# Kernel optimization log

Hardware: AMD Instinct MI355X
Metric: run time of the kernel (lower is better)

Reference implementation:

```python
import jax, jax.numpy as jnp
import numpy as np

V, D, B, S, T, MAXLEN = 32000, 256, 4, 512, 256, 512


def _gru(x, Wih, Whh, bih, bhh):
    """torch-style GRU over x:[B,L,Din] -> [B,L,D]. Weight rows ordered [r,z,n]."""
    Dh = Whh.shape[1]
    xW = x @ Wih.T + bih  # [B,L,3D] precompute input projections

    def step(h, xw):
        hW = h @ Whh.T + bhh
        xr, xz, xn = jnp.split(xw, 3, axis=-1)
        hr, hz, hn = jnp.split(hW, 3, axis=-1)
        r = jax.nn.sigmoid(xr + hr)
        z = jax.nn.sigmoid(xz + hz)
        n = jnp.tanh(xn + r * hn)
        h = (1.0 - z) * n + z * h
        return h, h

    h0 = jnp.zeros((x.shape[0], Dh), x.dtype)
    _, ys = jax.lax.scan(step, h0, jnp.swapaxes(xW, 0, 1))
    return jnp.swapaxes(ys, 0, 1)


def setup_inputs() -> dict:
    key = jax.random.key(0)
    ks = jax.random.split(key, 24)

    def n(k, shape, scale=0.02):
        return (jax.random.normal(k, shape, jnp.float32) * scale).astype(jnp.float32)

    inp = {
        "src": jax.random.randint(ks[0], (B, S), 0, V),
        "tgt": jax.random.randint(ks[1], (B, T), 0, V),
        "emb": n(ks[2], (V, D)),
        "pos": n(ks[3], (MAXLEN, D)),
        # encoder forward direction
        "ef_wih": n(ks[4], (3 * D, D)), "ef_whh": n(ks[5], (3 * D, D)),
        "ef_bih": n(ks[6], (3 * D,)), "ef_bhh": n(ks[7], (3 * D,)),
        # encoder backward direction
        "eb_wih": n(ks[8], (3 * D, D)), "eb_whh": n(ks[9], (3 * D, D)),
        "eb_bih": n(ks[10], (3 * D,)), "eb_bhh": n(ks[11], (3 * D,)),
        # decoder
        "d_wih": n(ks[12], (3 * D, D)), "d_whh": n(ks[13], (3 * D, D)),
        "d_bih": n(ks[14], (3 * D,)), "d_bhh": n(ks[15], (3 * D,)),
        "Wq": n(ks[16], (D, D)),
        "Wk": n(ks[17], (D, 2 * D)),
        "Wgen": n(ks[18], (V, 3 * D)), "bgen": n(ks[19], (V,)),
        "Wgate": n(ks[20], (1, 3 * D)), "bgate": n(ks[21], (1,)),
    }
    return inp


def reference(src, tgt, emb, pos,
              ef_wih, ef_whh, ef_bih, ef_bhh,
              eb_wih, eb_whh, eb_bih, eb_bhh,
              d_wih, d_whh, d_bih, d_bhh,
              Wq, Wk, Wgen, bgen, Wgate, bgate):
    b, s = src.shape
    t = tgt.shape[1]
    d = emb.shape[1]
    v = emb.shape[0]

    src_emb = emb[src] + pos[:s][None]          # [B,S,D]
    enc_f = _gru(src_emb, ef_wih, ef_whh, ef_bih, ef_bhh)
    enc_b = _gru(src_emb[:, ::-1], eb_wih, eb_whh, eb_bih, eb_bhh)[:, ::-1]
    enc_out = jnp.concatenate([enc_f, enc_b], axis=-1)  # [B,S,2D]

    tgt_emb = emb[tgt] + pos[:t][None]
    dec_out = _gru(tgt_emb, d_wih, d_whh, d_bih, d_bhh)  # [B,T,D]

    Q = dec_out @ Wq.T                           # [B,T,D]
    K = enc_out @ Wk.T                           # [B,S,D]
    scores = jnp.einsum('btd,bsd->bts', Q, K) / jnp.sqrt(jnp.asarray(d, jnp.float32))
    pos_probs = jax.nn.softmax(scores, axis=-1)  # [B,T,S]

    # copy distribution: scatter attention mass into vocab buckets (== one_hot bmm)
    P_copy = jnp.zeros((b, t, v), pos_probs.dtype).at[
        jnp.arange(b)[:, None, None],
        jnp.arange(t)[None, :, None],
        src[:, None, :],
    ].add(pos_probs)

    ctx_f = jnp.einsum('bts,bsd->btd', pos_probs, enc_f)
    ctx_b = jnp.einsum('bts,bsd->btd', pos_probs, enc_b)
    combined = jnp.concatenate([dec_out, ctx_f, ctx_b], axis=-1)  # [B,T,3D]

    P_gen = jax.nn.softmax(combined @ Wgen.T + bgen, axis=-1)     # [B,T,V]
    gate = jax.nn.sigmoid(combined @ Wgate.T + bgate)             # [B,T,1]
    return gate * P_gen + (1.0 - gate) * P_copy
```

## Files before the change

kernel.cpp:

```cpp
#include <hip/hip_runtime.h>
#include <hip/hip_bf16.h>
#include <math.h>

#define VV   32000
#define DIM  256
#define BB   4
#define SS   512
#define TT   256
#define D2   512
#define D3   768

typedef __attribute__((ext_vector_type(8))) short s16x8;
typedef __attribute__((ext_vector_type(4))) float f32x4;

__device__ __forceinline__ float rcp_(float x) { return __builtin_amdgcn_rcpf(x); }
__device__ __forceinline__ float sigmoidf_(float x) { return rcp_(1.0f + __expf(-x)); }
__device__ __forceinline__ float sigmoid_p(float x) { return 1.0f / (1.0f + __expf(-x)); }
__device__ __forceinline__ float tanh_p(float x) {
    float e2 = __expf(2.0f * x);
    return (e2 - 1.0f) / (e2 + 1.0f);
}
__device__ __forceinline__ short f2bf(float f) {
    unsigned u = __float_as_uint(f);
    u += 0x7FFFu + ((u >> 16) & 1u);
    return (short)(u >> 16);
}
__device__ __forceinline__ float bf2f(short s) {
    return __uint_as_float(((unsigned)(unsigned short)s) << 16);
}

#define BAR_LGKM() asm volatile("s_waitcnt lgkmcnt(0)\n\ts_barrier" ::: "memory")

struct PDesc {
    const int* tok;
    const float* Wt;
    const float* bias;
    float* C;
    int M;
    int lmask;
};

__global__ __launch_bounds__(512) void k_proj(const float* __restrict__ emb,
                                              const float* __restrict__ pos,
                                              PDesc p0, PDesc p1, PDesc p2) {
    PDesc p = (blockIdx.z == 0) ? p0 : ((blockIdx.z == 1) ? p1 : p2);
    int brow = blockIdx.y * 256;
    if (brow >= p.M) return;
    int bcol = blockIdx.x * 128;

    __shared__ __align__(16) short As[256 * 32];
    __shared__ __align__(16) short Bs[128 * 32];
    int tid = threadIdx.x;
    int lane = tid & 63, wv = tid >> 6;
    int wm = wv >> 1, wn = wv & 1;
    const int ll = lane & 15, lh = lane >> 4;

    f32x4 acc[4][4];
#pragma unroll
    for (int i = 0; i < 4; i++)
#pragma unroll
        for (int j = 0; j < 4; j++) acc[i][j] = (f32x4){0.f, 0.f, 0.f, 0.f};

    const int ar = tid >> 1, ak = (tid & 1) * 16;
    const int br = tid >> 2, bk = (tid & 3) * 8;
    const int grow = brow + ar;
    const float* erow = emb + (size_t)p.tok[grow] * DIM;
    const float* prow = pos + (size_t)(grow & p.lmask) * DIM;

    for (int k0 = 0; k0 < DIM; k0 += 32) {
        float4 a0 = *(const float4*)(erow + k0 + ak);
        float4 a1 = *(const float4*)(erow + k0 + ak + 4);
        float4 a2 = *(const float4*)(erow + k0 + ak + 8);
        float4 a3 = *(const float4*)(erow + k0 + ak + 12);
        float4 q0 = *(const float4*)(prow + k0 + ak);
        float4 q1 = *(const float4*)(prow + k0 + ak + 4);
        float4 q2 = *(const float4*)(prow + k0 + ak + 8);
        float4 q3 = *(const float4*)(prow + k0 + ak + 12);
        const float* bp = &p.Wt[(size_t)(bcol + br) * DIM + k0 + bk];
        float4 b0 = *(const float4*)bp;
        float4 b1 = *(const float4*)(bp + 4);
        s16x8 va0, va1, vb;
        va0[0] = f2bf(a0.x + q0.x); va0[1] = f2bf(a0.y + q0.y);
        va0[2] = f2bf(a0.z + q0.z); va0[3] = f2bf(a0.w + q0.w);
        va0[4] = f2bf(a1.x + q1.x); va0[5] = f2bf(a1.y + q1.y);
        va0[6] = f2bf(a1.z + q1.z); va0[7] = f2bf(a1.w + q1.w);
        va1[0] = f2bf(a2.x + q2.x); va1[1] = f2bf(a2.y + q2.y);
        va1[2] = f2bf(a2.z + q2.z); va1[3] = f2bf(a2.w + q2.w);
        va1[4] = f2bf(a3.x + q3.x); va1[5] = f2bf(a3.y + q3.y);
        va1[6] = f2bf(a3.z + q3.z); va1[7] = f2bf(a3.w + q3.w);
        vb[0] = f2bf(b0.x); vb[1] = f2bf(b0.y); vb[2] = f2bf(b0.z); vb[3] = f2bf(b0.w);
        vb[4] = f2bf(b1.x); vb[5] = f2bf(b1.y); vb[6] = f2bf(b1.z); vb[7] = f2bf(b1.w);

        __syncthreads();
        *(s16x8*)&As[ar * 32 + ak] = va0;
        *(s16x8*)&As[ar * 32 + ak + 8] = va1;
        *(s16x8*)&Bs[br * 32 + bk] = vb;
        __syncthreads();

        s16x8 af[4], bf[4];
#pragma unroll
        for (int mt = 0; mt < 4; ++mt)
            af[mt] = *(const s16x8*)&As[(wm * 64 + mt * 16 + ll) * 32 + lh * 8];
#pragma unroll
        for (int nt = 0; nt < 4; ++nt)
            bf[nt] = *(const s16x8*)&Bs[(wn * 64 + nt * 16 + ll) * 32 + lh * 8];
#pragma unroll
        for (int mt = 0; mt < 4; ++mt)
#pragma unroll
            for (int nt = 0; nt < 4; ++nt)
                acc[mt][nt] = __builtin_amdgcn_mfma_f32_16x16x32_bf16(af[mt], bf[nt], acc[mt][nt], 0, 0, 0);
    }

#pragma unroll
    for (int mt = 0; mt < 4; ++mt) {
        int row = brow + wm * 64 + mt * 16 + lh * 4;
#pragma unroll
        for (int nt = 0; nt < 4; ++nt) {
            int col = bcol + wn * 64 + nt * 16 + ll;
            float bv = p.bias[col];
#pragma unroll
            for (int q = 0; q < 4; ++q)
                p.C[(size_t)(row + q) * D3 + col] = acc[mt][nt][q] + bv;
        }
    }
}

struct QDesc {
    const float* A; int K;
    const float* Bt;
    float* C;
    int M;
};

__global__ __launch_bounds__(512) void k_qk(QDesc q0d, QDesc q1d) {
    QDesc p = (blockIdx.z == 0) ? q0d : q1d;
    int brow = blockIdx.y * 256;
    if (brow >= p.M) return;
    int bcol = blockIdx.x * 128;
    const int K = p.K;

    __shared__ __align__(16) short As[256 * 32];
    __shared__ __align__(16) short Bs[128 * 32];
    int tid = threadIdx.x;
    int lane = tid & 63, wv = tid >> 6;
    int wm = wv >> 1, wn = wv & 1;
    const int ll = lane & 15, lh = lane >> 4;

    f32x4 acc[4][4];
#pragma unroll
    for (int i = 0; i < 4; i++)
#pragma unroll
        for (int j = 0; j < 4; j++) acc[i][j] = (f32x4){0.f, 0.f, 0.f, 0.f};

    const int ar = tid >> 1, ak = (tid & 1) * 16;
    const int br = tid >> 2, bk = (tid & 3) * 8;

    for (int k0 = 0; k0 < K; k0 += 32) {
        const float* ap = &p.A[(size_t)(brow + ar) * K + k0 + ak];
        float4 a0 = *(const float4*)ap;
        float4 a1 = *(const float4*)(ap + 4);
        float4 a2 = *(const float4*)(ap + 8);
        float4 a3 = *(const float4*)(ap + 12);
        const float* bp = &p.Bt[(size_t)(bcol + br) * K + k0 + bk];
        float4 b0 = *(const float4*)bp;
        float4 b1 = *(const float4*)(bp + 4);
        s16x8 va0, va1, vb;
        va0[0] = f2bf(a0.x); va0[1] = f2bf(a0.y); va0[2] = f2bf(a0.z); va0[3] = f2bf(a0.w);
        va0[4] = f2bf(a1.x); va0[5] = f2bf(a1.y); va0[6] = f2bf(a1.z); va0[7] = f2bf(a1.w);
        va1[0] = f2bf(a2.x); va1[1] = f2bf(a2.y); va1[2] = f2bf(a2.z); va1[3] = f2bf(a2.w);
        va1[4] = f2bf(a3.x); va1[5] = f2bf(a3.y); va1[6] = f2bf(a3.z); va1[7] = f2bf(a3.w);
        vb[0] = f2bf(b0.x); vb[1] = f2bf(b0.y); vb[2] = f2bf(b0.z); vb[3] = f2bf(b0.w);
        vb[4] = f2bf(b1.x); vb[5] = f2bf(b1.y); vb[6] = f2bf(b1.z); vb[7] = f2bf(b1.w);

        __syncthreads();
        *(s16x8*)&As[ar * 32 + ak] = va0;
        *(s16x8*)&As[ar * 32 + ak + 8] = va1;
        *(s16x8*)&Bs[br * 32 + bk] = vb;
        __syncthreads();

        s16x8 af[4], bf[4];
#pragma unroll
        for (int mt = 0; mt < 4; ++mt)
            af[mt] = *(const s16x8*)&As[(wm * 64 + mt * 16 + ll) * 32 + lh * 8];
#pragma unroll
        for (int nt = 0; nt < 4; ++nt)
            bf[nt] = *(const s16x8*)&Bs[(wn * 64 + nt * 16 + ll) * 32 + lh * 8];
#pragma unroll
        for (int mt = 0; mt < 4; ++mt)
#pragma unroll
            for (int nt = 0; nt < 4; ++nt)
                acc[mt][nt] = __builtin_amdgcn_mfma_f32_16x16x32_bf16(af[mt], bf[nt], acc[mt][nt], 0, 0, 0);
    }

#pragma unroll
    for (int mt = 0; mt < 4; ++mt) {
        int row = brow + wm * 64 + mt * 16 + lh * 4;
#pragma unroll
        for (int nt = 0; nt < 4; ++nt) {
            int col = bcol + wn * 64 + nt * 16 + ll;
#pragma unroll
            for (int q = 0; q < 4; ++q)
                p.C[(size_t)(row + q) * DIM + col] = acc[mt][nt][q];
        }
    }
}

#define HSTRIDE 576
#define HBUF    (4 * HSTRIDE)
#define NCVT8   ((size_t)VV * D3 / 8)

__global__ __launch_bounds__(512, 2) void k_gru(const float* __restrict__ ef_x,
                                                const float* __restrict__ eb_x,
                                                const float* __restrict__ d_x,
                                                const float* __restrict__ ef_whh, const float* __restrict__ ef_bhh,
                                                const float* __restrict__ eb_whh, const float* __restrict__ eb_bhh,
                                                const float* __restrict__ d_whh, const float* __restrict__ d_bhh,
                                                float* __restrict__ enc_out,
                                                float* __restrict__ dec_out,
                                                const float* __restrict__ wgen,
                                                short* __restrict__ wgen_bf,
                                                float* __restrict__ rowsum,
                                                int do_cvt) {
    int tid = threadIdx.x;
    int bid = blockIdx.x;

    if (bid >= 3) {
        int cb = bid - 3;
        if (cb == 0) { rowsum[tid] = 0.0f; rowsum[tid + 512] = 0.0f; }
        if (do_cvt) {
            size_t i = (size_t)cb * 512 + tid;
            if (i < NCVT8) {
                const float4* p = (const float4*)(wgen + i * 8);
                float4 a = p[0], b4 = p[1];
                s16x8 v;
                v[0] = f2bf(a.x); v[1] = f2bf(a.y); v[2] = f2bf(a.z); v[3] = f2bf(a.w);
                v[4] = f2bf(b4.x); v[5] = f2bf(b4.y); v[6] = f2bf(b4.z); v[7] = f2bf(b4.w);
                *(s16x8*)(wgen_bf + i * 8) = v;
            }
        }
        return;
    }

    __shared__ __align__(16) char hb[2 * HBUF];
    int dir = bid;
    const float *xw, *Whh, *bhh;
    int L;
    if (dir == 0)      { xw = ef_x; Whh = ef_whh; bhh = ef_bhh; L = SS; }
    else if (dir == 1) { xw = eb_x; Whh = eb_whh; bhh = eb_bhh; L = SS; }
    else               { xw = d_x;  Whh = d_whh;  bhh = d_bhh;  L = TT; }

    const int wv = tid >> 6;
    const int lane = tid & 63;
    const int jj = lane & 15;
    const int hi = lane >> 4;
    const int b = hi;

    if (tid < 288) {
        f32x4 z = {0.f, 0.f, 0.f, 0.f};
        *(f32x4*)(hb + tid * 16) = z;
    }

    s16x8 wf[3][2][8];
#pragma unroll
    for (int g = 0; g < 3; ++g)
#pragma unroll
        for (int t = 0; t < 2; ++t) {
            const int nrow = g * 256 + wv * 32 + t * 16 + jj;
            const float* wp = Whh + (size_t)nrow * 256 + hi * 8;
#pragma unroll
            for (int sk = 0; sk < 8; ++sk) {
                float4 w0 = *(const float4*)(wp + sk * 32);
                float4 w1 = *(const float4*)(wp + sk * 32 + 4);
                s16x8 v;
                v[0] = f2bf(w0.x); v[1] = f2bf(w0.y); v[2] = f2bf(w0.z); v[3] = f2bf(w0.w);
                v[4] = f2bf(w1.x); v[5] = f2bf(w1.y); v[6] = f2bf(w1.z); v[7] = f2bf(w1.w);
                wf[g][t][sk] = v;
            }
        }

    const int j0 = wv * 32 + jj, j1 = j0 + 16;
    const float br0 = bhh[j0], bz0 = bhh[256 + j0], bn0 = bhh[512 + j0];
    const float br1 = bhh[j1], bz1 = bhh[256 + j1], bn1 = bhh[512 + j1];

    const int arow = jj >> 2;
    const int abase = arow * HSTRIDE + hi * 16;
    const int wo0 = b * HSTRIDE + 2 * j0;
    const int wo1 = b * HSTRIDE + 2 * j1;

    const int s0 = (dir == 1) ? (L - 1) : 0;
    const int sst = (dir == 1) ? -1 : 1;
    const float* xq = xw + ((size_t)b * L + s0) * D3 + j0;
    float* op;
    int ostride;
    if (dir == 2) { op = dec_out + ((size_t)b * TT + s0) * DIM + j0; ostride = sst * DIM; }
    else          { op = enc_out + ((size_t)b * SS + s0) * D2 + (dir == 1 ? DIM : 0) + j0; ostride = sst * D2; }
    const int xstride = sst * D3;

    float c0 = xq[0], c1 = xq[256], c2 = xq[512], c3 = xq[16], c4 = xq[272], c5 = xq[528];

    float h0 = 0.f, h1 = 0.f;
    int cur = 0;
    __syncthreads();

    for (int st = 0; st < L; ++st) {
        xq += xstride;
        float n0 = xq[0], n1 = xq[256], n2 = xq[512], n3 = xq[16], n4 = xq[272], n5 = xq[528];

        const char* hcur = hb + cur * HBUF;
        f32x4 a00 = {0.f, 0.f, 0.f, 0.f}, a01 = a00, a10 = a00, a11 = a00, a20 = a00, a21 = a00;
#pragma unroll
        for (int sk = 0; sk < 8; ++sk) {
            s16x8 af = *(const s16x8*)(hcur + abase + 64 * sk);
            a00 = __builtin_amdgcn_mfma_f32_16x16x32_bf16(af, wf[0][0][sk], a00, 0, 0, 0);
            a01 = __builtin_amdgcn_mfma_f32_16x16x32_bf16(af, wf[0][1][sk], a01, 0, 0, 0);
            a10 = __builtin_amdgcn_mfma_f32_16x16x32_bf16(af, wf[1][0][sk], a10, 0, 0, 0);
            a11 = __builtin_amdgcn_mfma_f32_16x16x32_bf16(af, wf[1][1][sk], a11, 0, 0, 0);
            a20 = __builtin_amdgcn_mfma_f32_16x16x32_bf16(af, wf[2][0][sk], a20, 0, 0, 0);
            a21 = __builtin_amdgcn_mfma_f32_16x16x32_bf16(af, wf[2][1][sk], a21, 0, 0, 0);
        }

        float r0 = sigmoid_p(c0 + a00[0] + br0);
        float z0 = sigmoid_p(c1 + a10[0] + bz0);
        float nn0 = tanh_p(c2 + r0 * (a20[0] + bn0));
        h0 = (1.f - z0) * nn0 + z0 * h0;
        float r1 = sigmoid_p(c3 + a01[0] + br1);
        float z1 = sigmoid_p(c4 + a11[0] + bz1);
        float nn1 = tanh_p(c5 + r1 * (a21[0] + bn1));
        h1 = (1.f - z1) * nn1 + z1 * h1;

        char* hnxt = hb + (cur ^ 1) * HBUF;
        *(short*)(hnxt + wo0) = f2bf(h0);
        *(short*)(hnxt + wo1) = f2bf(h1);
        op[0] = h0;
        op[16] = h1;
        BAR_LGKM();

        cur ^= 1;
        c0 = n0; c1 = n1; c2 = n2; c3 = n3; c4 = n4; c5 = n5;
        op += ostride;
    }
}

__global__ __launch_bounds__(512) void k_attn(const float* __restrict__ Qb,
                                              const float* __restrict__ Kb,
                                              const float* __restrict__ enc_out,
                                              const float* __restrict__ dec_out,
                                              const float* __restrict__ Wgate,
                                              const float* __restrict__ bgate,
                                              float* __restrict__ probs,
                                              short* __restrict__ cmb,
                                              float* __restrict__ gate) {
    __shared__ float q[DIM];
    __shared__ float sc[SS];
    __shared__ float red[512];
    __shared__ float par[2][2][DIM];
    int row = blockIdx.x;
    int b = row >> 8;
    int tid = threadIdx.x;

    if (tid < DIM) q[tid] = Qb[(size_t)row * DIM + tid];
    __syncthreads();

    const float scale = 0.0625f;
    {
        const float* kr = Kb + ((size_t)b * SS + tid) * DIM;
        float acc = 0.0f;
        for (int k = 0; k < DIM; k += 4) {
            float4 k4 = *(const float4*)&kr[k];
            acc += k4.x * q[k] + k4.y * q[k + 1] + k4.z * q[k + 2] + k4.w * q[k + 3];
        }
        sc[tid] = acc * scale;
    }
    __syncthreads();

    red[tid] = sc[tid];
    __syncthreads();
    for (int o = 256; o > 0; o >>= 1) {
        if (tid < o) red[tid] = fmaxf(red[tid], red[tid + o]);
        __syncthreads();
    }
    float m = red[0];
    __syncthreads();

    float e0 = __expf(sc[tid] - m);
    sc[tid] = e0;
    red[tid] = e0;
    __syncthreads();
    for (int o = 256; o > 0; o >>= 1) {
        if (tid < o) red[tid] += red[tid + o];
        __syncthreads();
    }
    float inv = rcp_(red[0]);
    __syncthreads();

    sc[tid] *= inv;
    probs[(size_t)row * SS + tid] = sc[tid];
    __syncthreads();

    {
        int d = tid & 255, sh = tid >> 8;
        float accf = 0.0f, accb = 0.0f;
        const float* ep = enc_out + ((size_t)b * SS + sh * 256) * D2 + d;
        const float* pp = &sc[sh * 256];
        for (int s = 0; s < 256; s++) {
            float p = pp[s];
            accf += p * ep[(size_t)s * D2];
            accb += p * ep[(size_t)s * D2 + DIM];
        }
        par[sh][0][d] = accf;
        par[sh][1][d] = accb;
    }
    __syncthreads();

    if (tid < DIM) {
        float af = par[0][0][tid] + par[1][0][tid];
        float ab = par[0][1][tid] + par[1][1][tid];
        float dv = dec_out[(size_t)row * DIM + tid];
        cmb[(size_t)row * D3 + tid] = f2bf(dv);
        cmb[(size_t)row * D3 + DIM + tid] = f2bf(af);
        cmb[(size_t)row * D3 + 2 * DIM + tid] = f2bf(ab);
        red[tid] = dv * Wgate[tid] + af * Wgate[DIM + tid] + ab * Wgate[2 * DIM + tid];
    }
    __syncthreads();
    for (int o = 128; o > 0; o >>= 1) {
        if (tid < o) red[tid] += red[tid + o];
        __syncthreads();
    }
    if (tid == 0) gate[row] = sigmoidf_(red[0] + bgate[0]);
}

#define GEN_PROLOGUE()                                                      \
    __shared__ __align__(16) short As[256 * 32];                            \
    __shared__ __align__(16) short Bs[128 * 32];                            \
    int tid = threadIdx.x;                                                  \
    int lane = tid & 63, wv = tid >> 6;                                     \
    int wm = wv >> 1, wn = wv & 1;                                          \
    int brow = blockIdx.y * 256, bcol = blockIdx.x * 128;                   \
    f32x4 acc[4][4];                                                        \
    _Pragma("unroll") for (int i = 0; i < 4; i++)                           \
        _Pragma("unroll") for (int j = 0; j < 4; j++)                       \
            acc[i][j] = (f32x4){0.f, 0.f, 0.f, 0.f};                        \
    const int ca0 = tid, ca1 = tid + 512, cb = tid;                         \
    const int ll = lane & 15, lh = lane >> 4;

#define GEN_MAINLOOP(LOAD_B)                                                \
    for (int k0 = 0; k0 < D3; k0 += 32) {                                   \
        s16x8 va0 = *(const s16x8*)&A[(size_t)(brow + (ca0 >> 2)) * D3 + k0 + (ca0 & 3) * 8]; \
        s16x8 va1 = *(const s16x8*)&A[(size_t)(brow + (ca1 >> 2)) * D3 + k0 + (ca1 & 3) * 8]; \
        s16x8 vb; LOAD_B;                                                   \
        __syncthreads();                                                    \
        *(s16x8*)&As[ca0 * 8] = va0;                                        \
        *(s16x8*)&As[ca1 * 8] = va1;                                        \
        *(s16x8*)&Bs[cb * 8] = vb;                                          \
        __syncthreads();                                                    \
        s16x8 af[4], bf[4];                                                 \
        _Pragma("unroll") for (int mt = 0; mt < 4; ++mt)                    \
            af[mt] = *(const s16x8*)&As[(wm * 64 + mt * 16 + ll) * 32 + lh * 8]; \
        _Pragma("unroll") for (int nt = 0; nt < 4; ++nt)                    \
            bf[nt] = *(const s16x8*)&Bs[(wn * 64 + nt * 16 + ll) * 32 + lh * 8]; \
        _Pragma("unroll") for (int mt = 0; mt < 4; ++mt)                    \
            _Pragma("unroll") for (int nt = 0; nt < 4; ++nt)                \
                acc[mt][nt] = __builtin_amdgcn_mfma_f32_16x16x32_bf16(af[mt], bf[nt], acc[mt][nt], 0, 0, 0); \
    }

#define LOADB_BF  vb = *(const s16x8*)&Bbf[(size_t)(bcol + (cb >> 2)) * D3 + k0 + (cb & 3) * 8]
#define LOADB_F32 do {                                                      \
        const float* bp = &Bw[(size_t)(bcol + (cb >> 2)) * D3 + k0 + (cb & 3) * 8]; \
        float4 b0 = *(const float4*)bp; float4 b1 = *(const float4*)(bp + 4); \
        vb[0] = f2bf(b0.x); vb[1] = f2bf(b0.y); vb[2] = f2bf(b0.z); vb[3] = f2bf(b0.w); \
        vb[4] = f2bf(b1.x); vb[5] = f2bf(b1.y); vb[6] = f2bf(b1.z); vb[7] = f2bf(b1.w); } while (0)

#define GEN_ROWSUM(EXPR)                                                    \
    _Pragma("unroll") for (int mt = 0; mt < 4; ++mt)                        \
        _Pragma("unroll") for (int q = 0; q < 4; ++q) {                     \
            float se = (EXPR);                                              \
            _Pragma("unroll") for (int off = 1; off < 16; off <<= 1)        \
                se += __shfl_xor(se, off);                                  \
            if (ll == 0) atomicAdd(&rowsum[brow + wm * 64 + mt * 16 + lh * 4 + q], se); \
        }

__global__ __launch_bounds__(512) void k_genb(const short* __restrict__ A,
                                              const short* __restrict__ Bbf,
                                              const float* __restrict__ bias,
                                              short* __restrict__ C16,
                                              float* __restrict__ rowsum) {
    GEN_PROLOGUE();
    GEN_MAINLOOP(LOADB_BF);
    short lr[4][4][4];
#pragma unroll
    for (int nt = 0; nt < 4; ++nt) {
        float bv = bias[bcol + wn * 64 + nt * 16 + ll];
#pragma unroll
        for (int mt = 0; mt < 4; ++mt)
#pragma unroll
            for (int q = 0; q < 4; ++q) lr[mt][nt][q] = f2bf(acc[mt][nt][q] + bv);
    }
#pragma unroll
    for (int mt = 0; mt < 4; ++mt) {
        int row = brow + wm * 64 + mt * 16 + lh * 4;
#pragma unroll
        for (int nt = 0; nt < 4; ++nt) {
            int col = bcol + wn * 64 + nt * 16 + ll;
#pragma unroll
            for (int q = 0; q < 4; ++q)
                C16[(size_t)(row + q) * VV + col] = lr[mt][nt][q];
        }
    }
    GEN_ROWSUM(__expf(bf2f(lr[mt][0][q])) + __expf(bf2f(lr[mt][1][q])) +
               __expf(bf2f(lr[mt][2][q])) + __expf(bf2f(lr[mt][3][q])));
}

__global__ __launch_bounds__(512) void k_gen_bf(const short* __restrict__ A,
                                                const short* __restrict__ Bbf,
                                                const float* __restrict__ bias,
                                                float* __restrict__ C,
                                                float* __restrict__ rowsum) {
    GEN_PROLOGUE();
    GEN_MAINLOOP(LOADB_BF);
#pragma unroll
    for (int nt = 0; nt < 4; ++nt) {
        float bv = bias[bcol + wn * 64 + nt * 16 + ll];
#pragma unroll
        for (int mt = 0; mt < 4; ++mt)
#pragma unroll
            for (int q = 0; q < 4; ++q) acc[mt][nt][q] += bv;
    }
#pragma unroll
    for (int mt = 0; mt < 4; ++mt) {
        int row = brow + wm * 64 + mt * 16 + lh * 4;
#pragma unroll
        for (int nt = 0; nt < 4; ++nt) {
            int col = bcol + wn * 64 + nt * 16 + ll;
#pragma unroll
            for (int q = 0; q < 4; ++q)
                C[(size_t)(row + q) * VV + col] = acc[mt][nt][q];
        }
    }
    GEN_ROWSUM(__expf(acc[mt][0][q]) + __expf(acc[mt][1][q]) +
               __expf(acc[mt][2][q]) + __expf(acc[mt][3][q]));
}

__global__ __launch_bounds__(512) void k_gen(const short* __restrict__ A,
                                             const float* __restrict__ Bw,
                                             const float* __restrict__ bias,
                                             float* __restrict__ C,
                                             float* __restrict__ rowsum) {
    GEN_PROLOGUE();
    GEN_MAINLOOP(LOADB_F32);
#pragma unroll
    for (int nt = 0; nt < 4; ++nt) {
        float bv = bias[bcol + wn * 64 + nt * 16 + ll];
#pragma unroll
        for (int mt = 0; mt < 4; ++mt)
#pragma unroll
            for (int q = 0; q < 4; ++q) acc[mt][nt][q] += bv;
    }
#pragma unroll
    for (int mt = 0; mt < 4; ++mt) {
        int row = brow + wm * 64 + mt * 16 + lh * 4;
#pragma unroll
        for (int nt = 0; nt < 4; ++nt) {
            int col = bcol + wn * 64 + nt * 16 + ll;
#pragma unroll
            for (int q = 0; q < 4; ++q)
                C[(size_t)(row + q) * VV + col] = acc[mt][nt][q];
        }
    }
    GEN_ROWSUM(__expf(acc[mt][0][q]) + __expf(acc[mt][1][q]) +
               __expf(acc[mt][2][q]) + __expf(acc[mt][3][q]));
}

__global__ __launch_bounds__(256) void k_finsc_bf(const int* __restrict__ src,
                                                  const float* __restrict__ probs,
                                                  const float* __restrict__ gate,
                                                  const float* __restrict__ rowsum,
                                                  const short* __restrict__ L16,
                                                  float* __restrict__ out) {
    int row = blockIdx.x;
    int b = row >> 8;
    int tid = threadIdx.x;
    float g = gate[row];
    float inv = g / rowsum[row];
    const short* lp = L16 + (size_t)row * VV;
    float* op = out + (size_t)row * VV;

    for (int i = tid; i < VV / 8; i += 256) {
        s16x8 l8 = *(const s16x8*)&lp[i * 8];
        float4 o0, o1;
        o0.x = __expf(bf2f(l8[0])) * inv; o0.y = __expf(bf2f(l8[1])) * inv;
        o0.z = __expf(bf2f(l8[2])) * inv; o0.w = __expf(bf2f(l8[3])) * inv;
        o1.x = __expf(bf2f(l8[4])) * inv; o1.y = __expf(bf2f(l8[5])) * inv;
        o1.z = __expf(bf2f(l8[6])) * inv; o1.w = __expf(bf2f(l8[7])) * inv;
        *(float4*)&op[i * 8] = o0;
        *(float4*)&op[i * 8 + 4] = o1;
    }
    __syncthreads();

    float og = 1.0f - g;
#pragma unroll
    for (int h = 0; h < 2; ++h) {
        int s = tid + h * 256;
        float val = og * probs[(size_t)row * SS + s];
        atomicAdd(&op[src[b * SS + s]], val);
    }
}

__global__ __launch_bounds__(256) void k_finsc(const int* __restrict__ src,
                                               const float* __restrict__ probs,
                                               const float* __restrict__ gate,
                                               const float* __restrict__ rowsum,
                                               float* __restrict__ out) {
    int row = blockIdx.x;
    int b = row >> 8;
    int tid = threadIdx.x;
    float g = gate[row];
    float inv = g / rowsum[row];
    float* op = out + (size_t)row * VV;

    for (int i = tid; i < VV / 4; i += 256) {
        float4 l = *(const float4*)&op[i * 4];
        l.x = __expf(l.x) * inv;
        l.y = __expf(l.y) * inv;
        l.z = __expf(l.z) * inv;
        l.w = __expf(l.w) * inv;
        *(float4*)&op[i * 4] = l;
    }
    __syncthreads();

    float og = 1.0f - g;
#pragma unroll
    for (int h = 0; h < 2; ++h) {
        int s = tid + h * 256;
        float val = og * probs[(size_t)row * SS + s];
        atomicAdd(&op[src[b * SS + s]], val);
    }
}

extern "C" void kernel_launch(void* const* d_in, const int* in_sizes, int n_in,
                              void* d_out, int out_size, void* d_ws, size_t ws_size,
                              hipStream_t stream) {
    const int*   src    = (const int*)d_in[0];
    const int*   tgt    = (const int*)d_in[1];
    const float* emb    = (const float*)d_in[2];
    const float* pos    = (const float*)d_in[3];
    const float* ef_wih = (const float*)d_in[4];
    const float* ef_whh = (const float*)d_in[5];
    const float* ef_bih = (const float*)d_in[6];
    const float* ef_bhh = (const float*)d_in[7];
    const float* eb_wih = (const float*)d_in[8];
    const float* eb_whh = (const float*)d_in[9];
    const float* eb_bih = (const float*)d_in[10];
    const float* eb_bhh = (const float*)d_in[11];
    const float* d_wih  = (const float*)d_in[12];
    const float* d_whh  = (const float*)d_in[13];
    const float* d_bih  = (const float*)d_in[14];
    const float* d_bhh  = (const float*)d_in[15];
    const float* Wq     = (const float*)d_in[16];
    const float* Wk     = (const float*)d_in[17];
    const float* Wgen   = (const float*)d_in[18];
    const float* bgen   = (const float*)d_in[19];
    const float* Wgate  = (const float*)d_in[20];
    const float* bgate  = (const float*)d_in[21];
    float* out = (float*)d_out;
    float* ws  = (float*)d_ws;

    float* ef_x     = ws;
    float* eb_x     = ef_x + (size_t)BB * SS * D3;
    float* d_x      = eb_x + (size_t)BB * SS * D3;
    float* enc_out  = d_x + (size_t)BB * TT * D3;
    float* dec_out  = enc_out + (size_t)BB * SS * D2;
    float* Qb       = dec_out + (size_t)BB * TT * DIM;
    float* Kb       = Qb + (size_t)BB * TT * DIM;
    float* probs    = Kb + (size_t)BB * SS * DIM;
    short* cmb_bf   = (short*)(probs + (size_t)BB * TT * SS);
    float* gate     = (float*)(cmb_bf + (size_t)BB * TT * D3);
    float* rowsum   = gate + 1024;
    short* wgen_bf  = (short*)(rowsum + 1024);
    short* logit_bf = wgen_bf + (size_t)VV * D3;
    const bool use_bf  = ws_size >= (size_t)((char*)(wgen_bf + (size_t)VV * D3) - (char*)d_ws);
    const bool use_lbf = ws_size >= (size_t)((char*)(logit_bf + (size_t)VV * BB * TT) - (char*)d_ws);

    {
        PDesc e0 = {src, ef_wih, ef_bih, ef_x, BB * SS, SS - 1};
        PDesc e1 = {src, eb_wih, eb_bih, eb_x, BB * SS, SS - 1};
        PDesc e2 = {tgt, d_wih, d_bih, d_x, BB * TT, TT - 1};
        k_proj<<<dim3(D3 / 128, BB * SS / 256, 3), 512, 0, stream>>>(emb, pos, e0, e1, e2);
    }

    {
        int ncvtb = (int)((NCVT8 + 511) / 512);
        k_gru<<<3 + ncvtb, 512, 0, stream>>>(ef_x, eb_x, d_x,
                                             ef_whh, ef_bhh, eb_whh, eb_bhh, d_whh, d_bhh,
                                             enc_out, dec_out,
                                             Wgen, wgen_bf, rowsum, use_bf ? 1 : 0);
    }

    {
        QDesc q0 = {dec_out, DIM, Wq, Qb, BB * TT};
        QDesc q1 = {enc_out, D2, Wk, Kb, BB * SS};
        k_qk<<<dim3(DIM / 128, BB * SS / 256, 2), 512, 0, stream>>>(q0, q1);
    }

    k_attn<<<BB * TT, 512, 0, stream>>>(Qb, Kb, enc_out, dec_out, Wgate, bgate,
                                        probs, cmb_bf, gate);

    dim3 gg(VV / 128, (BB * TT) / 256);
    if (use_lbf) {
        k_genb<<<gg, 512, 0, stream>>>(cmb_bf, wgen_bf, bgen, logit_bf, rowsum);
        k_finsc_bf<<<BB * TT, 256, 0, stream>>>(src, probs, gate, rowsum, logit_bf, out);
    } else if (use_bf) {
        k_gen_bf<<<gg, 512, 0, stream>>>(cmb_bf, wgen_bf, bgen, out, rowsum);
        k_finsc<<<BB * TT, 256, 0, stream>>>(src, probs, gate, rowsum, out);
    } else {
        k_gen<<<gg, 512, 0, stream>>>(cmb_bf, Wgen, bgen, out, rowsum);
        k_finsc<<<BB * TT, 256, 0, stream>>>(src, probs, gate, rowsum, out);
    }
}
```

Before: 1.074 ms.

## Batch four query rows per attention block and double-buffer generator GEMM LDS tiles

The attention kernel now handles four decoder rows per block, so each K row and enc_out element loaded from global memory is reused across four queries, and the softmax reductions are split into per-row 128-wide trees. Separately, the vocab-projection GEMM main loop is double-buffered in shared memory, prefetching the next K-slice into registers while MFMAs run on the current one, with one barrier per iteration instead of two. This trades doubled LDS usage and more registers for less global traffic and more overlap.

```diff
diff --git a/kernel.cpp b/kernel.cpp
--- a/kernel.cpp
+++ b/kernel.cpp
@@ -341,6 +341,7 @@
     }
 }
 
+#define TBR 4
 __global__ __launch_bounds__(512) void k_attn(const float* __restrict__ Qb,
                                               const float* __restrict__ Kb,
                                               const float* __restrict__ enc_out,
@@ -350,88 +351,118 @@
                                               float* __restrict__ probs,
                                               short* __restrict__ cmb,
                                               float* __restrict__ gate) {
-    __shared__ float q[DIM];
-    __shared__ float sc[SS];
+    __shared__ float q[TBR][DIM];
+    __shared__ float sc[TBR][SS];
     __shared__ float red[512];
-    __shared__ float par[2][2][DIM];
-    int row = blockIdx.x;
-    int b = row >> 8;
+    __shared__ float par[2][2][TBR][DIM];
+    __shared__ float gred[TBR][DIM];
+    int row0 = blockIdx.x * TBR;
+    int b = row0 >> 8;
     int tid = threadIdx.x;
 
-    if (tid < DIM) q[tid] = Qb[(size_t)row * DIM + tid];
+#pragma unroll
+    for (int p = 0; p < 2; ++p) {
+        int idx = tid + p * 512;
+        q[idx >> 8][idx & 255] = Qb[(size_t)(row0 + (idx >> 8)) * DIM + (idx & 255)];
+    }
     __syncthreads();
 
     const float scale = 0.0625f;
     {
         const float* kr = Kb + ((size_t)b * SS + tid) * DIM;
-        float acc = 0.0f;
+        float a0 = 0.f, a1 = 0.f, a2 = 0.f, a3 = 0.f;
         for (int k = 0; k < DIM; k += 4) {
             float4 k4 = *(const float4*)&kr[k];
-            acc += k4.x * q[k] + k4.y * q[k + 1] + k4.z * q[k + 2] + k4.w * q[k + 3];
-        }
-        sc[tid] = acc * scale;
-    }
-    __syncthreads();
-
-    red[tid] = sc[tid];
-    __syncthreads();
-    for (int o = 256; o > 0; o >>= 1) {
-        if (tid < o) red[tid] = fmaxf(red[tid], red[tid + o]);
+            a0 += k4.x * q[0][k] + k4.y * q[0][k + 1] + k4.z * q[0][k + 2] + k4.w * q[0][k + 3];
+            a1 += k4.x * q[1][k] + k4.y * q[1][k + 1] + k4.z * q[1][k + 2] + k4.w * q[1][k + 3];
+            a2 += k4.x * q[2][k] + k4.y * q[2][k + 1] + k4.z * q[2][k + 2] + k4.w * q[2][k + 3];
+            a3 += k4.x * q[3][k] + k4.y * q[3][k + 1] + k4.z * q[3][k + 2] + k4.w * q[3][k + 3];
+        }
+        sc[0][tid] = a0 * scale; sc[1][tid] = a1 * scale;
+        sc[2][tid] = a2 * scale; sc[3][tid] = a3 * scale;
+    }
+    __syncthreads();
+
+    const int rr = tid >> 7, ri = tid & 127;
+    red[tid] = fmaxf(fmaxf(sc[rr][ri], sc[rr][ri + 128]),
+                     fmaxf(sc[rr][ri + 256], sc[rr][ri + 384]));
+    __syncthreads();
+    for (int o = 64; o > 0; o >>= 1) {
+        if (ri < o) red[tid] = fmaxf(red[tid], red[tid + o]);
         __syncthreads();
     }
-    float m = red[0];
-    __syncthreads();
-
-    float e0 = __expf(sc[tid] - m);
-    sc[tid] = e0;
-    red[tid] = e0;
-    __syncthreads();
-    for (int o = 256; o > 0; o >>= 1) {
-        if (tid < o) red[tid] += red[tid + o];
+    float m = red[rr << 7];
+    __syncthreads();
+
+    float e0 = __expf(sc[rr][ri] - m);
+    float e1 = __expf(sc[rr][ri + 128] - m);
+    float e2 = __expf(sc[rr][ri + 256] - m);
+    float e3 = __expf(sc[rr][ri + 384] - m);
+    sc[rr][ri] = e0; sc[rr][ri + 128] = e1; sc[rr][ri + 256] = e2; sc[rr][ri + 384] = e3;
+    red[tid] = e0 + e1 + e2 + e3;
+    __syncthreads();
+    for (int o = 64; o > 0; o >>= 1) {
+        if (ri < o) red[tid] += red[tid + o];
         __syncthreads();
     }
-    float inv = rcp_(red[0]);
-    __syncthreads();
-
-    sc[tid] *= inv;
-    probs[(size_t)row * SS + tid] = sc[tid];
-    __syncthreads();
+    float inv = rcp_(red[rr << 7]);
+    __syncthreads();
+    sc[rr][ri] *= inv; sc[rr][ri + 128] *= inv;
+    sc[rr][ri + 256] *= inv; sc[rr][ri + 384] *= inv;
+    __syncthreads();
+
+#pragma unroll
+    for (int p = 0; p < 4; ++p) {
+        int idx = tid + p * 512;
+        probs[(size_t)(row0 + (idx >> 9)) * SS + (idx & 511)] = sc[idx >> 9][idx & 511];
+    }
 
     {
         int d = tid & 255, sh = tid >> 8;
-        float accf = 0.0f, accb = 0.0f;
+        float f0 = 0.f, f1 = 0.f, f2 = 0.f, f3 = 0.f;
+        float g0 = 0.f, g1 = 0.f, g2 = 0.f, g3 = 0.f;
         const float* ep = enc_out + ((size_t)b * SS + sh * 256) * D2 + d;
-        const float* pp = &sc[sh * 256];
-        for (int s = 0; s < 256; s++) {
-            float p = pp[s];
-            accf += p * ep[(size_t)s * D2];
-            accb += p * ep[(size_t)s * D2 + DIM];
-        }
-        par[sh][0][d] = accf;
-        par[sh][1][d] = accb;
+        for (int s = 0; s < 256; ++s) {
+            float ef_ = ep[(size_t)s * D2];
+            float eb_ = ep[(size_t)s * D2 + DIM];
+            int s2 = sh * 256 + s;
+            float p0 = sc[0][s2], p1 = sc[1][s2], p2 = sc[2][s2], p3 = sc[3][s2];
+            f0 += p0 * ef_; f1 += p1 * ef_; f2 += p2 * ef_; f3 += p3 * ef_;
+            g0 += p0 * eb_; g1 += p1 * eb_; g2 += p2 * eb_; g3 += p3 * eb_;
+        }
+        par[sh][0][0][d] = f0; par[sh][0][1][d] = f1; par[sh][0][2][d] = f2; par[sh][0][3][d] = f3;
+        par[sh][1][0][d] = g0; par[sh][1][1][d] = g1; par[sh][1][2][d] = g2; par[sh][1][3][d] = g3;
     }
     __syncthreads();
 
     if (tid < DIM) {
-        float af = par[0][0][tid] + par[1][0][tid];
-        float ab = par[0][1][tid] + par[1][1][tid];
-        float dv = dec_out[(size_t)row * DIM + tid];
-        cmb[(size_t)row * D3 + tid] = f2bf(dv);
-        cmb[(size_t)row * D3 + DIM + tid] = f2bf(af);
-        cmb[(size_t)row * D3 + 2 * DIM + tid] = f2bf(ab);
-        red[tid] = dv * Wgate[tid] + af * Wgate[DIM + tid] + ab * Wgate[2 * DIM + tid];
-    }
-    __syncthreads();
-    for (int o = 128; o > 0; o >>= 1) {
-        if (tid < o) red[tid] += red[tid + o];
+        float w0 = Wgate[tid], w1 = Wgate[DIM + tid], w2 = Wgate[2 * DIM + tid];
+#pragma unroll
+        for (int r = 0; r < TBR; ++r) {
+            float af = par[0][0][r][tid] + par[1][0][r][tid];
+            float ab = par[0][1][r][tid] + par[1][1][r][tid];
+            float dv = dec_out[(size_t)(row0 + r) * DIM + tid];
+            size_t cb = (size_t)(row0 + r) * D3;
+            cmb[cb + tid] = f2bf(dv);
+            cmb[cb + DIM + tid] = f2bf(af);
+            cmb[cb + 2 * DIM + tid] = f2bf(ab);
+            gred[r][tid] = dv * w0 + af * w1 + ab * w2;
+        }
+    }
+    __syncthreads();
+
+    red[tid] = gred[rr][ri] + gred[rr][ri + 128];
+    __syncthreads();
+    for (int o = 64; o > 0; o >>= 1) {
+        if (ri < o) red[tid] += red[tid + o];
         __syncthreads();
     }
-    if (tid == 0) gate[row] = sigmoidf_(red[0] + bgate[0]);
+    if (ri == 0) gate[row0 + rr] = sigmoidf_(red[rr << 7] + bgate[0]);
 }
 
 #define GEN_PROLOGUE()                                                      \
-    __shared__ __align__(16) short As[256 * 32];                            \
-    __shared__ __align__(16) short Bs[128 * 32];                            \
+    __shared__ __align__(16) short As[2][256 * 32];                         \
+    __shared__ __align__(16) short Bs[2][128 * 32];                         \
     int tid = threadIdx.x;                                                  \
     int lane = tid & 63, wv = tid >> 6;                                     \
     int wm = wv >> 1, wn = wv & 1;                                          \
@@ -443,32 +474,48 @@
     const int ca0 = tid, ca1 = tid + 512, cb = tid;                         \
     const int ll = lane & 15, lh = lane >> 4;
 
-#define GEN_MAINLOOP(LOAD_B)                                                \
+#define LOADA(k)                                                            \
+    va0 = *(const s16x8*)&A[(size_t)(brow + (ca0 >> 2)) * D3 + (k) + (ca0 & 3) * 8]; \
+    va1 = *(const s16x8*)&A[(size_t)(brow + (ca1 >> 2)) * D3 + (k) + (ca1 & 3) * 8];
+
+#define LOADB_BF(k)                                                         \
+    vb = *(const s16x8*)&Bbf[(size_t)(bcol + (cb >> 2)) * D3 + (k) + (cb & 3) * 8]
+
+#define LOADB_F32(k) do {                                                   \
+        const float* bp = &Bw[(size_t)(bcol + (cb >> 2)) * D3 + (k) + (cb & 3) * 8]; \
+        float4 b0 = *(const float4*)bp; float4 b1 = *(const float4*)(bp + 4); \
+        vb[0] = f2bf(b0.x); vb[1] = f2bf(b0.y); vb[2] = f2bf(b0.z); vb[3] = f2bf(b0.w); \
+        vb[4] = f2bf(b1.x); vb[5] = f2bf(b1.y); vb[6] = f2bf(b1.z); vb[7] = f2bf(b1.w); } while (0)
+
+#define GEN_MAIN2(LOADB)                                                    \
+    {                                                                       \
+        s16x8 va0, va1, vb;                                                 \
+        LOADA(0); LOADB(0);                                                 \
+        *(s16x8*)&As[0][ca0 * 8] = va0;                                     \
+        *(s16x8*)&As[0][ca1 * 8] = va1;                                     \
+        *(s16x8*)&Bs[0][cb * 8] = vb;                                       \
+        __syncthreads();                                                    \
+    }                                                                       \
     for (int k0 = 0; k0 < D3; k0 += 32) {                                   \
-        s16x8 va0 = *(const s16x8*)&A[(size_t)(brow + (ca0 >> 2)) * D3 + k0 + (ca0 & 3) * 8]; \
-        s16x8 va1 = *(const s16x8*)&A[(size_t)(brow + (ca1 >> 2)) * D3 + k0 + (ca1 & 3) * 8]; \
-        s16x8 vb; LOAD_B;                                                   \
-        __syncthreads();                                                    \
-        *(s16x8*)&As[ca0 * 8] = va0;                                        \
-        *(s16x8*)&As[ca1 * 8] = va1;                                        \
-        *(s16x8*)&Bs[cb * 8] = vb;                                          \
-        __syncthreads();                                                    \
+        const int cur = (k0 >> 5) & 1;                                      \
+        const int kn = k0 + 32;                                             \
+        s16x8 va0, va1, vb;                                                 \
+        if (kn < D3) { LOADA(kn); LOADB(kn); }                              \
         s16x8 af[4], bf[4];                                                 \
         _Pragma("unroll") for (int mt = 0; mt < 4; ++mt)                    \
-            af[mt] = *(const s16x8*)&As[(wm * 64 + mt * 16 + ll) * 32 + lh * 8]; \
+            af[mt] = *(const s16x8*)&As[cur][(wm * 64 + mt * 16 + ll) * 32 + lh * 8]; \
         _Pragma("unroll") for (int nt = 0; nt < 4; ++nt)                    \
-            bf[nt] = *(const s16x8*)&Bs[(wn * 64 + nt * 16 + ll) * 32 + lh * 8]; \
+            bf[nt] = *(const s16x8*)&Bs[cur][(wn * 64 + nt * 16 + ll) * 32 + lh * 8]; \
         _Pragma("unroll") for (int mt = 0; mt < 4; ++mt)                    \
             _Pragma("unroll") for (int nt = 0; nt < 4; ++nt)                \
                 acc[mt][nt] = __builtin_amdgcn_mfma_f32_16x16x32_bf16(af[mt], bf[nt], acc[mt][nt], 0, 0, 0); \
-    }
-
-#define LOADB_BF  vb = *(const s16x8*)&Bbf[(size_t)(bcol + (cb >> 2)) * D3 + k0 + (cb & 3) * 8]
-#define LOADB_F32 do {                                                      \
-        const float* bp = &Bw[(size_t)(bcol + (cb >> 2)) * D3 + k0 + (cb & 3) * 8]; \
-        float4 b0 = *(const float4*)bp; float4 b1 = *(const float4*)(bp + 4); \
-        vb[0] = f2bf(b0.x); vb[1] = f2bf(b0.y); vb[2] = f2bf(b0.z); vb[3] = f2bf(b0.w); \
-        vb[4] = f2bf(b1.x); vb[5] = f2bf(b1.y); vb[6] = f2bf(b1.z); vb[7] = f2bf(b1.w); } while (0)
+        if (kn < D3) {                                                      \
+            *(s16x8*)&As[cur ^ 1][ca0 * 8] = va0;                           \
+            *(s16x8*)&As[cur ^ 1][ca1 * 8] = va1;                           \
+            *(s16x8*)&Bs[cur ^ 1][cb * 8] = vb;                             \
+        }                                                                   \
+        __syncthreads();                                                    \
+    }
 
 #define GEN_ROWSUM(EXPR)                                                    \
     _Pragma("unroll") for (int mt = 0; mt < 4; ++mt)                        \
@@ -485,7 +532,7 @@
                                               short* __restrict__ C16,
                                               float* __restrict__ rowsum) {
     GEN_PROLOGUE();
-    GEN_MAINLOOP(LOADB_BF);
+    GEN_MAIN2(LOADB_BF);
     short lr[4][4][4];
 #pragma unroll
     for (int nt = 0; nt < 4; ++nt) {
@@ -516,7 +563,7 @@
                                                 float* __restrict__ C,
                                                 float* __restrict__ rowsum) {
     GEN_PROLOGUE();
-    GEN_MAINLOOP(LOADB_BF);
+    GEN_MAIN2(LOADB_BF);
 #pragma unroll
     for (int nt = 0; nt < 4; ++nt) {
         float bv = bias[bcol + wn * 64 + nt * 16 + ll];
@@ -546,7 +593,7 @@
                                              float* __restrict__ C,
                                              float* __restrict__ rowsum) {
     GEN_PROLOGUE();
-    GEN_MAINLOOP(LOADB_F32);
+    GEN_MAIN2(LOADB_F32);
 #pragma unroll
     for (int nt = 0; nt < 4; ++nt) {
         float bv = bias[bcol + wn * 64 + nt * 16 + ll];
@@ -701,8 +748,8 @@
         k_qk<<<dim3(DIM / 128, BB * SS / 256, 2), 512, 0, stream>>>(q0, q1);
     }
 
-    k_attn<<<BB * TT, 512, 0, stream>>>(Qb, Kb, enc_out, dec_out, Wgate, bgate,
-                                        probs, cmb_bf, gate);
+    k_attn<<<BB * TT / TBR, 512, 0, stream>>>(Qb, Kb, enc_out, dec_out, Wgate, bgate,
+                                              probs, cmb_bf, gate);
 
     dim3 gg(VV / 128, (BB * TT) / 256);
     if (use_lbf) {
```

New measurement: 1.106 ms. 3.0% more time.
